# Optimization experiments

Hardware: AMD Instinct MI355X
Metric: run time of the kernel (lower is better)

Reference implementation:

```python
import math
import jax, jax.numpy as jnp
import numpy as np

N_VARS = 10
K_MAX = 2
D = 32
B = 262144


def _fourier_emb(t, k_max=K_MAX):
    # [B, 1 + 2*k_max]: [1, cos(w t), sin(w t), cos(2 w t), sin(2 w t)]
    omega = 2.0 * math.pi
    feats = [jnp.ones_like(t)]
    for k in range(1, k_max + 1):
        feats.append(jnp.cos(k * omega * t))
        feats.append(jnp.sin(k * omega * t))
    return jnp.stack(feats, axis=-1)


def _make_mask(n_vars=N_VARS, mask_mode='th_only'):
    mask = jnp.eye(n_vars, dtype=jnp.float32)
    if mask_mode == 'th_only':
        mask = mask.at[:, 0].set(1.0)
        mask = mask.at[:, 1].set(1.0)
    else:
        mask = jnp.ones((n_vars, n_vars), dtype=jnp.float32)
    return mask


def setup_inputs() -> dict:
    key = jax.random.key(0)
    ks = jax.random.split(key, 8)
    x = jax.random.normal(ks[0], (B, N_VARS), dtype=jnp.float32)
    t_years = jax.random.uniform(ks[1], (B,), dtype=jnp.float32)
    n_basis = 1 + 2 * K_MAX
    # xavier-uniform-ish init for L_basis (fan over last two dims)
    limit = math.sqrt(6.0 / (N_VARS + N_VARS))
    L_basis = jax.random.uniform(ks[2], (n_basis, N_VARS, N_VARS), dtype=jnp.float32,
                                 minval=-limit, maxval=limit)
    wq = jax.random.normal(ks[3], (D,), dtype=jnp.float32)
    wk = jax.random.normal(ks[4], (D,), dtype=jnp.float32)
    wv = jax.random.normal(ks[5], (D,), dtype=jnp.float32)
    wo = jax.random.normal(ks[6], (D,), dtype=jnp.float32)
    alpha_w = 0.1 * jax.random.normal(ks[7], (n_basis,), dtype=jnp.float32)
    return {"x": x, "t_years": t_years, "L_basis": L_basis,
            "wq": wq, "wk": wk, "wv": wv, "wo": wo, "alpha_w": alpha_w}


def reference(x, t_years, L_basis, wq, wk, wv, wo, alpha_w):
    emb = _fourier_emb(t_years)                       # [B, K]
    L_t = jnp.einsum('bk,kuv->buv', emb, L_basis)      # [B, V, V]
    dxdt = jnp.einsum('buv,bv->bu', L_t, x)            # [B, V]

    # tokens: x[..., None] with Linear(1, d, bias=False) == outer product with weight vector
    Q = x[..., None] * wq                              # [B, V, D]
    K = x[..., None] * wk
    Vv = x[..., None] * wv

    scale = 1.0 / math.sqrt(D)
    scores = jnp.einsum('bvd,bud->bvu', Q, K) * scale  # [B, V, V]
    mask = _make_mask()
    scores = jnp.where(mask[None] < 0.5, -1e9, scores)
    attn = jax.nn.softmax(scores, axis=-1)
    O = jnp.einsum('bvu,bud->bvd', attn, Vv)           # [B, V, D]
    out = jnp.einsum('bvd,d->bv', O, wo)               # Wo: Linear(d,1,bias=False)

    alpha = jax.nn.sigmoid(emb @ alpha_w)              # [B]
    return dxdt + out * alpha[:, None]
```

## Files before the change

kernel.cpp:

```cpp
#include <hip/hip_runtime.h>
#include <math.h>

constexpr int NV  = 10;
constexpr int NB  = 5;
constexpr int DD  = 32;
constexpr int BLK = 256;

#define CONST_AS __attribute__((address_space(4)))
__device__ __forceinline__ const CONST_AS float* cptr(const float* p) {
    return (const CONST_AS float*)(unsigned long long)p;
}

__global__ __launch_bounds__(BLK) void nxro_fused(
    const float* __restrict__ x,
    const float* __restrict__ t,
    const float* __restrict__ L,
    const float* __restrict__ wq,
    const float* __restrict__ wk,
    const float* __restrict__ wv,
    const float* __restrict__ wo,
    const float* __restrict__ aw,
    float* __restrict__ out,
    int B)
{
    __shared__ float4 sstage4[BLK * NV / 4];
    float* sstage = reinterpret_cast<float*>(sstage4);

    const int tid = threadIdx.x;
    const long long base  = (long long)blockIdx.x * BLK;
    const long long nelem = (long long)B * NV;

    const CONST_AS float* Lc  = cptr(L);
    const CONST_AS float* wqc = cptr(wq);
    const CONST_AS float* wkc = cptr(wk);
    const CONST_AS float* wvc = cptr(wv);
    const CONST_AS float* woc = cptr(wo);
    const CONST_AS float* awc = cptr(aw);

    float qk = 0.f, vo = 0.f;
    #pragma unroll
    for (int d = 0; d < DD; ++d) {
        qk = fmaf(wqc[d], wkc[d], qk);
        vo = fmaf(wvc[d], woc[d], vo);
    }
    const float c = qk * 0.17677669529663687f;
    const float g = vo;

    {
        const float4* xg = reinterpret_cast<const float4*>(x + base * NV);
        const long long n4 = (nelem - base * NV) / 4;
        #pragma unroll
        for (int i = tid; i < BLK * NV / 4; i += BLK)
            sstage4[i] = (i < n4) ? xg[i] : make_float4(0.f, 0.f, 0.f, 0.f);
    }
    __syncthreads();

    const long long b = base + tid;
    const bool active = (b < (long long)B);
    if (active) {
        float xv[NV];
        #pragma unroll
        for (int v = 0; v < NV; ++v) xv[v] = sstage[tid * NV + v];
        const float tt = t[b];

        const float t2 = tt + tt;
        const float emb[NB] = {
            1.f,
            __builtin_amdgcn_cosf(tt),
            __builtin_amdgcn_sinf(tt),
            __builtin_amdgcn_cosf(t2),
            __builtin_amdgcn_sinf(t2)
        };

        float dxdt[NV];
        #pragma unroll
        for (int u = 0; u < NV; ++u) dxdt[u] = 0.f;
        #pragma unroll
        for (int k = 0; k < NB; ++k) {
            const float ek = emb[k];
            #pragma unroll
            for (int u = 0; u < NV; ++u) {
                const CONST_AS float* Lr = Lc + (k * NV + u) * NV;
                float acc = Lr[0] * xv[0];
                #pragma unroll
                for (int v = 1; v < NV; ++v)
                    acc = fmaf(Lr[v], xv[v], acc);
                dxdt[u] = fmaf(ek, acc, dxdt[u]);
            }
        }

        float z = 0.f;
        #pragma unroll
        for (int k = 0; k < NB; ++k) z = fmaf(emb[k], awc[k], z);
        const float alpha = 1.f / (1.f + __expf(-z));
        const float ga = g * alpha;

        const float x0 = xv[0], x1 = xv[1];
        float res[NV];
        #pragma unroll
        for (int v = 0; v < NV; ++v) {
            const float s0 = xv[v] * x0 * c;
            const float s1 = xv[v] * x1 * c;
            float w;
            if (v < 2) {
                const float m = fmaxf(s0, s1);
                const float e0 = __expf(s0 - m), e1 = __expf(s1 - m);
                w = fmaf(e0, x0, e1 * x1) / (e0 + e1);
            } else {
                const float sv = xv[v] * xv[v] * c;
                const float m = fmaxf(fmaxf(s0, s1), sv);
                const float e0 = __expf(s0 - m), e1 = __expf(s1 - m),
                            ev = __expf(sv - m);
                w = fmaf(e0, x0, fmaf(e1, x1, ev * xv[v])) / (e0 + e1 + ev);
            }
            res[v] = fmaf(w, ga, dxdt[v]);
        }
        #pragma unroll
        for (int v = 0; v < NV; ++v) sstage[tid * NV + v] = res[v];
    }
    __syncthreads();

    {
        float4* og = reinterpret_cast<float4*>(out + base * NV);
        const long long n4 = (nelem - base * NV) / 4;
        #pragma unroll
        for (int i = tid; i < BLK * NV / 4; i += BLK)
            if (i < n4) og[i] = sstage4[i];
    }
}

extern "C" void kernel_launch(void* const* d_in, const int* in_sizes, int n_in,
                              void* d_out, int out_size, void* d_ws, size_t ws_size,
                              hipStream_t stream) {
    const float* x  = (const float*)d_in[0];
    const float* t  = (const float*)d_in[1];
    const float* L  = (const float*)d_in[2];
    const float* wq = (const float*)d_in[3];
    const float* wk = (const float*)d_in[4];
    const float* wv = (const float*)d_in[5];
    const float* wo = (const float*)d_in[6];
    const float* aw = (const float*)d_in[7];
    float* out = (float*)d_out;
    const int B = in_sizes[1];

    const int grid = (B + BLK - 1) / BLK;
    nxro_fused<<<grid, BLK, 0, stream>>>(x, t, L, wq, wk, wv, wo, aw, out, B);
}
```

Baseline: 16.05 us.

## Drop LDS staging, load rows directly, precompute emb*x, shuffle-reduce weight dots

Removes the shared-memory staging and both block barriers, so each thread now reads its x row and writes its output row directly as float2 accesses. The weight dot products move from a serial 32-step scalar loop to a wavefront shuffle reduction. The L contraction is restructured to precompute emb*x products and stream L as float4 loads with one FMA per element, which avoids the extra per-basis multiply. Divisions become hardware reciprocals. The trade-off is that uncoalesced strided row accesses (40-byte stride) replace the coalesced float4 block copies, and L now comes through vector loads instead of scalar constant loads.

```diff
diff --git a/kernel.cpp b/kernel.cpp
--- a/kernel.cpp
+++ b/kernel.cpp
@@ -3,7 +3,6 @@
 
 constexpr int NV  = 10;
 constexpr int NB  = 5;
-constexpr int DD  = 32;
 constexpr int BLK = 256;
 
 #define CONST_AS __attribute__((address_space(4)))
@@ -23,109 +22,106 @@
     float* __restrict__ out,
     int B)
 {
-    __shared__ float4 sstage4[BLK * NV / 4];
-    float* sstage = reinterpret_cast<float*>(sstage4);
+    const int tid  = threadIdx.x;
+    const int lane = tid & 63;
 
-    const int tid = threadIdx.x;
-    const long long base  = (long long)blockIdx.x * BLK;
-    const long long nelem = (long long)B * NV;
+    float pa, pb;
+    if (lane < 32) { pa = wq[lane];      pb = wk[lane];      }
+    else           { pa = wv[lane - 32]; pb = wo[lane - 32]; }
+    float dotv = pa * pb;
+    #pragma unroll
+    for (int m = 16; m >= 1; m >>= 1)
+        dotv += __shfl_xor(dotv, m, 64);
+    const float c = __shfl(dotv, 0, 64) * 0.17677669529663687f;
+    const float g = __shfl(dotv, 32, 64);
 
-    const CONST_AS float* Lc  = cptr(L);
-    const CONST_AS float* wqc = cptr(wq);
-    const CONST_AS float* wkc = cptr(wk);
-    const CONST_AS float* wvc = cptr(wv);
-    const CONST_AS float* woc = cptr(wo);
+    const long long b = (long long)blockIdx.x * BLK + tid;
+    if (b >= (long long)B) return;
+
+    const float tt = t[b];
+    const float t2 = tt + tt;
+    const float emb1 = __builtin_amdgcn_cosf(tt);
+    const float emb2 = __builtin_amdgcn_sinf(tt);
+    const float emb3 = __builtin_amdgcn_cosf(t2);
+    const float emb4 = __builtin_amdgcn_sinf(t2);
+
+    float xv[NV];
+    {
+        const float2* xr = reinterpret_cast<const float2*>(x + b * NV);
+        #pragma unroll
+        for (int i = 0; i < 5; ++i) {
+            const float2 p = xr[i];
+            xv[2 * i] = p.x; xv[2 * i + 1] = p.y;
+        }
+    }
+
+    float zz[NB - 1][NV];
+    #pragma unroll
+    for (int v = 0; v < NV; ++v) {
+        zz[0][v] = emb1 * xv[v];
+        zz[1][v] = emb2 * xv[v];
+        zz[2][v] = emb3 * xv[v];
+        zz[3][v] = emb4 * xv[v];
+    }
+
+    float dxdt[NV];
+    #pragma unroll
+    for (int u = 0; u < NV; ++u) dxdt[u] = 0.f;
+    {
+        const float4* __restrict__ L4 = reinterpret_cast<const float4*>(L);
+        #pragma unroll
+        for (int f = 0; f < 125; ++f) {
+            const float4 q = L4[f];
+            #pragma unroll
+            for (int cc = 0; cc < 4; ++cc) {
+                const int e = 4 * f + cc;
+                const int k = e / 100;
+                const int u = (e / 10) % 10;
+                const int v = e % 10;
+                const float qc = (cc == 0) ? q.x : (cc == 1) ? q.y
+                               : (cc == 2) ? q.z : q.w;
+                const float zj = (k == 0) ? xv[v] : zz[k - 1][v];
+                dxdt[u] = fmaf(qc, zj, dxdt[u]);
+            }
+        }
+    }
+
     const CONST_AS float* awc = cptr(aw);
+    float zs = awc[0];
+    zs = fmaf(emb1, awc[1], zs);
+    zs = fmaf(emb2, awc[2], zs);
+    zs = fmaf(emb3, awc[3], zs);
+    zs = fmaf(emb4, awc[4], zs);
+    const float alpha = __builtin_amdgcn_rcpf(1.f + __expf(-zs));
+    const float ga = g * alpha;
 
-    float qk = 0.f, vo = 0.f;
+    const float x0 = xv[0], x1 = xv[1];
+    float res[NV];
     #pragma unroll
-    for (int d = 0; d < DD; ++d) {
-        qk = fmaf(wqc[d], wkc[d], qk);
-        vo = fmaf(wvc[d], woc[d], vo);
+    for (int v = 0; v < NV; ++v) {
+        const float s0 = xv[v] * x0 * c;
+        const float s1 = xv[v] * x1 * c;
+        float w;
+        if (v < 2) {
+            const float m = fmaxf(s0, s1);
+            const float e0 = __expf(s0 - m), e1 = __expf(s1 - m);
+            w = fmaf(e0, x0, e1 * x1) * __builtin_amdgcn_rcpf(e0 + e1);
+        } else {
+            const float sv = xv[v] * xv[v] * c;
+            const float m = fmaxf(fmaxf(s0, s1), sv);
+            const float e0 = __expf(s0 - m), e1 = __expf(s1 - m),
+                        ev = __expf(sv - m);
+            w = fmaf(e0, x0, fmaf(e1, x1, ev * xv[v]))
+                * __builtin_amdgcn_rcpf(e0 + e1 + ev);
+        }
+        res[v] = fmaf(w, ga, dxdt[v]);
     }
-    const float c = qk * 0.17677669529663687f;
-    const float g = vo;
 
     {
-        const float4* xg = reinterpret_cast<const float4*>(x + base * NV);
-        const long long n4 = (nelem - base * NV) / 4;
+        float2* orow = reinterpret_cast<float2*>(out + b * NV);
         #pragma unroll
-        for (int i = tid; i < BLK * NV / 4; i += BLK)
-            sstage4[i] = (i < n4) ? xg[i] : make_float4(0.f, 0.f, 0.f, 0.f);
-    }
-    __syncthreads();
-
-    const long long b = base + tid;
-    const bool active = (b < (long long)B);
-    if (active) {
-        float xv[NV];
-        #pragma unroll
-        for (int v = 0; v < NV; ++v) xv[v] = sstage[tid * NV + v];
-        const float tt = t[b];
-
-        const float t2 = tt + tt;
-        const float emb[NB] = {
-            1.f,
-            __builtin_amdgcn_cosf(tt),
-            __builtin_amdgcn_sinf(tt),
-            __builtin_amdgcn_cosf(t2),
-            __builtin_amdgcn_sinf(t2)
-        };
-
-        float dxdt[NV];
-        #pragma unroll
-        for (int u = 0; u < NV; ++u) dxdt[u] = 0.f;
-        #pragma unroll
-        for (int k = 0; k < NB; ++k) {
-            const float ek = emb[k];
-            #pragma unroll
-            for (int u = 0; u < NV; ++u) {
-                const CONST_AS float* Lr = Lc + (k * NV + u) * NV;
-                float acc = Lr[0] * xv[0];
-                #pragma unroll
-                for (int v = 1; v < NV; ++v)
-                    acc = fmaf(Lr[v], xv[v], acc);
-                dxdt[u] = fmaf(ek, acc, dxdt[u]);
-            }
-        }
-
-        float z = 0.f;
-        #pragma unroll
-        for (int k = 0; k < NB; ++k) z = fmaf(emb[k], awc[k], z);
-        const float alpha = 1.f / (1.f + __expf(-z));
-        const float ga = g * alpha;
-
-        const float x0 = xv[0], x1 = xv[1];
-        float res[NV];
-        #pragma unroll
-        for (int v = 0; v < NV; ++v) {
-            const float s0 = xv[v] * x0 * c;
-            const float s1 = xv[v] * x1 * c;
-            float w;
-            if (v < 2) {
-                const float m = fmaxf(s0, s1);
-                const float e0 = __expf(s0 - m), e1 = __expf(s1 - m);
-                w = fmaf(e0, x0, e1 * x1) / (e0 + e1);
-            } else {
-                const float sv = xv[v] * xv[v] * c;
-                const float m = fmaxf(fmaxf(s0, s1), sv);
-                const float e0 = __expf(s0 - m), e1 = __expf(s1 - m),
-                            ev = __expf(sv - m);
-                w = fmaf(e0, x0, fmaf(e1, x1, ev * xv[v])) / (e0 + e1 + ev);
-            }
-            res[v] = fmaf(w, ga, dxdt[v]);
-        }
-        #pragma unroll
-        for (int v = 0; v < NV; ++v) sstage[tid * NV + v] = res[v];
-    }
-    __syncthreads();
-
-    {
-        float4* og = reinterpret_cast<float4*>(out + base * NV);
-        const long long n4 = (nelem - base * NV) / 4;
-        #pragma unroll
-        for (int i = tid; i < BLK * NV / 4; i += BLK)
-            if (i < n4) og[i] = sstage4[i];
+        for (int i = 0; i < 5; ++i)
+            orow[i] = make_float2(res[2 * i], res[2 * i + 1]);
     }
 }
 
```

New measurement: 13.58 us. 1.18x faster.
